# Kernel tuning notes

Measured on AMD Instinct MI355X. Metric: run time of the kernel, lower is better.

The kernel has to match this reference:

```python
import jax, jax.numpy as jnp
import numpy as np

PROJ_DIM = 16384  # self.projDim / output_dim
THRESH = 1e-8     # self.thresh


def setup_inputs() -> dict:
    key = jax.random.key(0)
    k1, k2, k3, k4, k5 = jax.random.split(key, 5)
    B, C, H, W = 16, 2048, 14, 14
    x = jax.random.normal(k1, (B, C, H, W), dtype=jnp.float32)
    # count-sketch hash indices and Rademacher signs (fixed random params of CBP)
    h1 = jax.random.randint(k2, (C,), 0, PROJ_DIM, dtype=jnp.int32)
    h2 = jax.random.randint(k3, (C,), 0, PROJ_DIM, dtype=jnp.int32)
    w1 = (2 * jax.random.randint(k4, (C,), 0, 2) - 1).astype(jnp.float32)
    w2 = (2 * jax.random.randint(k5, (C,), 0, 2) - 1).astype(jnp.float32)
    return {"x": x, "w1": w1, "w2": w2, "h1": h1, "h2": h2}


def _count_sketch(xf, w, h):
    # xf: (N, C); scatter-add signed features into PROJ_DIM bins per location
    N = xf.shape[0]
    return jnp.zeros((N, PROJ_DIM), xf.dtype).at[:, h].add(xf * w)


def reference(x, w1, w2, h1, h2):
    B, C, H, W = x.shape
    # (B, C, H, W) -> (B*H*W, C): one feature vector per spatial location
    xf = x.transpose(0, 2, 3, 1).reshape(B * H * W, C)
    s1 = _count_sketch(xf, w1, h1)  # (N, D)
    s2 = _count_sketch(xf, w2, h2)  # (N, D)
    # circular convolution of the two sketches via FFT (real input -> rfft)
    y = jnp.fft.irfft(jnp.fft.rfft(s1, axis=-1) * jnp.fft.rfft(s2, axis=-1),
                      n=PROJ_DIM, axis=-1)  # (N, D)
    # sum-pool over spatial locations
    y = y.reshape(B, H * W, PROJ_DIM).sum(axis=1)  # (B, D)
    # signed sqrt + L2 normalization
    y = jnp.sign(y) * jnp.sqrt(jnp.abs(y) + THRESH)
    y = y / jnp.sqrt(jnp.sum(y * y, axis=-1, keepdims=True) + THRESH)
    return y  # (B, 16384), already flat as in torch.flatten(..., 1)
```

## Files before the change

kernel.cpp:

```cpp
#include <hip/hip_runtime.h>


#define D_PROJ 16384
#define C_CH   2048
#define HW_N   196
#define NKS    7
#define KPAD   (NKS * 32)
#define B_N    16
#define THREADS 512
#define NT     64
#define BUFS   6
#define AHEAD  4
#define ROWSH  448
#define FPSCALE 65536.0f
#define INVSCALE (1.0f / 65536.0f)

typedef short  short8 __attribute__((ext_vector_type(8)));
typedef float  f32x4  __attribute__((ext_vector_type(4)));
typedef int    i32x4  __attribute__((ext_vector_type(4)));

static __device__ inline unsigned short f2bf(float f) {
    union { float f; unsigned u; } a; a.f = f;
    unsigned u = a.u;
    return (unsigned short)((u + 0x7FFFu + ((u >> 16) & 1u)) >> 16);
}
static __device__ inline float bf2f(unsigned short h) {
    union { unsigned u; float f; } a; a.u = ((unsigned)h) << 16;
    return a.f;
}
static __device__ inline f32x4 mfma16(short8 a, short8 b, f32x4 c) {
    return __builtin_amdgcn_mfma_f32_16x16x32_bf16(a, b, c, 0, 0, 0);
}

static __device__ inline void lds_iadd(int* p, int v) {
    unsigned off = (unsigned)(uintptr_t)p;
    asm volatile("ds_add_u32 %0, %1" :: "v"(off), "v"(v) : "memory");
}
static __device__ inline void lds_fadd(float* p, float v) {
    unsigned off = (unsigned)(uintptr_t)p;
    asm volatile("ds_add_f32 %0, %1" :: "v"(off), "v"(v) : "memory");
}
static __device__ inline void lds_drain() {
    asm volatile("s_waitcnt lgkmcnt(0)" ::: "memory");
    __builtin_amdgcn_sched_barrier(0);
}

static __device__ inline int swz_off(int ks, int lo64, int sub16, int row7) {
    return (((ks << 7) | lo64 | (sub16 << 4)) ^ (row7 << 4));
}

__global__ __launch_bounds__(256)
void cbp_convert(const float* __restrict__ x, unsigned short* __restrict__ ws) {
    const int id = blockIdx.x * 256 + threadIdx.x;
    const int total = B_N * C_CH * (KPAD / 8);
    if (id >= total) return;
    const int row = id / (KPAD / 8);
    const int sub = id - row * (KPAD / 8);
    const int k0  = sub * 8;
    const int ks  = k0 >> 5;
    const int s16 = (k0 >> 3) & 3;

    const float* xr = x + (size_t)row * HW_N;
    float v[8];
    if (k0 + 8 <= HW_N) {
        f32x4 p0 = *(const f32x4*)(xr + k0);
        f32x4 p1 = *(const f32x4*)(xr + k0 + 4);
#pragma unroll
        for (int e = 0; e < 4; ++e) { v[e] = p0[e]; v[4 + e] = p1[e]; }
    } else {
#pragma unroll
        for (int e = 0; e < 8; ++e) {
            const int k = k0 + e;
            v[e] = (k < HW_N) ? xr[k] : 0.0f;
        }
    }
    short8 hv, lv;
#pragma unroll
    for (int e = 0; e < 8; ++e) {
        unsigned short h = f2bf(v[e]);
        hv[e] = (short)h;
        lv[e] = (short)f2bf(v[e] - bf2f(h));
    }
    char* rowB = (char*)ws + (size_t)row * (ROWSH * 2);
    const int r7 = row & 7;
    *(short8*)(rowB + swz_off(ks, 0,  s16, r7)) = hv;
    *(short8*)(rowB + swz_off(ks, 64, s16, r7)) = lv;
}

static __device__ inline void stage_issue(const unsigned short* __restrict__ src0,
                                          unsigned short* dst0, int wave, int lane) {
    if (lane < 56) {
#pragma unroll
        for (int hlf = 0; hlf < 2; ++hlf) {
            const int row = wave + hlf * 8;
            const unsigned short* s = src0 + (size_t)row * ROWSH + (size_t)lane * 8;
            unsigned short* d = dst0 + (size_t)row * ROWSH;
            __builtin_amdgcn_global_load_lds(
                (const __attribute__((address_space(1))) void*)s,
                (__attribute__((address_space(3))) void*)d, 16, 0, 0);
        }
    }
}

__global__ __launch_bounds__(THREADS, 2)
void cbp_gram10(const unsigned short* __restrict__ ws,
                const float* __restrict__ w1f,
                const float* __restrict__ w2f,
                const int*   __restrict__ h1,
                const int*   __restrict__ h2,
                int*         __restrict__ part) {
    __shared__ __align__(16) int hist[D_PROJ];
    __shared__ __align__(16) unsigned short stage[BUFS][16 * ROWSH];
    __shared__ float w2sh[1024];
    __shared__ int   h2sh[1024];

    const int id   = blockIdx.x;
    const int b    = ((id & 7) << 1) | ((id >> 3) & 1);
    const int rest = id >> 4;
    const int j0   = (rest & 1) * 1024;
    const int i0   = (rest >> 1) * 256;

    const int tid  = threadIdx.x;
    const int wave = tid >> 6;
    const int lane = tid & 63;
    const int l15  = lane & 15;
    const int lgrp = lane >> 4;
    const int r7s  = (l15 & 7) << 4;

    for (int t = tid; t < D_PROJ / 4; t += THREADS)
        ((i32x4*)hist)[t] = i32x4{0, 0, 0, 0};
    for (int t = tid; t < 1024; t += THREADS) {
        w2sh[t] = w2f[j0 + t];
        h2sh[t] = h2[j0 + t];
    }

    short8 ah[2][NKS], al[2][NKS];
    int    binr[2][4];
    float  s1r[2][4];
#pragma unroll
    for (int s = 0; s < 2; ++s) {
        const int irow = i0 + wave * 32 + s * 16 + l15;
        const char* rowA = (const char*)(ws + ((size_t)b * C_CH + irow) * ROWSH);
#pragma unroll
        for (int ks = 0; ks < NKS; ++ks) {
            ah[s][ks] = *(const short8*)(rowA + (((ks << 7) | (lgrp << 4)) ^ r7s));
            al[s][ks] = *(const short8*)(rowA + (((ks << 7) | 64 | (lgrp << 4)) ^ r7s));
        }
#pragma unroll
        for (int r = 0; r < 4; ++r) {
            const int ir = i0 + wave * 32 + s * 16 + lgrp * 4 + r;
            binr[s][r] = h1[ir];
            s1r[s][r]  = w1f[ir];
        }
    }

    const unsigned short* jbase = ws + ((size_t)b * C_CH + j0) * ROWSH;
#pragma unroll
    for (int p = 0; p < AHEAD; ++p)
        stage_issue(jbase + (size_t)p * 16 * ROWSH, stage[p], wave, lane);

    asm volatile("s_waitcnt lgkmcnt(0)\ns_barrier" ::: "memory");

    for (int t = 0; t < NT; ++t) {
        int tt = t + AHEAD; tt = (tt < NT) ? tt : (NT - 1);
        stage_issue(jbase + (size_t)tt * 16 * ROWSH, stage[(t + AHEAD) % BUFS], wave, lane);
        asm volatile("s_waitcnt vmcnt(8)" ::: "memory");
        __builtin_amdgcn_sched_barrier(0);
        asm volatile("s_barrier" ::: "memory");
        __builtin_amdgcn_sched_barrier(0);

        const char* srow = (const char*)&stage[t % BUFS][(size_t)l15 * ROWSH];
        f32x4 a0 = {0.f,0.f,0.f,0.f}, a1 = {0.f,0.f,0.f,0.f};
        f32x4 b0 = {0.f,0.f,0.f,0.f}, b1 = {0.f,0.f,0.f,0.f};
#pragma unroll
        for (int ks = 0; ks < NKS; ++ks) {
            const short8 bh = *(const short8*)(srow + (((ks << 7) | (lgrp << 4)) ^ r7s));
            const short8 bl = *(const short8*)(srow + (((ks << 7) | 64 | (lgrp << 4)) ^ r7s));
            if (ks & 1) {
                a1 = mfma16(ah[0][ks], bh, a1);  b1 = mfma16(ah[1][ks], bh, b1);
                a1 = mfma16(al[0][ks], bh, a1);  b1 = mfma16(al[1][ks], bh, b1);
                a1 = mfma16(ah[0][ks], bl, a1);  b1 = mfma16(ah[1][ks], bl, b1);
            } else {
                a0 = mfma16(ah[0][ks], bh, a0);  b0 = mfma16(ah[1][ks], bh, b0);
                a0 = mfma16(al[0][ks], bh, a0);  b0 = mfma16(al[1][ks], bh, b0);
                a0 = mfma16(ah[0][ks], bl, a0);  b0 = mfma16(ah[1][ks], bl, b0);
            }
        }
        const float w2vs = w2sh[t * 16 + l15] * FPSCALE;
        const int   h2v  = h2sh[t * 16 + l15];
        const f32x4 g0 = a0 + a1;
        const f32x4 g1 = b0 + b1;
#pragma unroll
        for (int r = 0; r < 4; ++r) {
            int bin = binr[0][r] + h2v;
            if (bin >= D_PROJ) bin -= D_PROJ;
            const int iv = (int)rintf(g0[r] * (s1r[0][r] * w2vs));
            lds_iadd(&hist[bin], iv);
        }
#pragma unroll
        for (int r = 0; r < 4; ++r) {
            int bin = binr[1][r] + h2v;
            if (bin >= D_PROJ) bin -= D_PROJ;
            const int iv = (int)rintf(g1[r] * (s1r[1][r] * w2vs));
            lds_iadd(&hist[bin], iv);
        }
    }

    lds_drain();
    __syncthreads();
    int* pslot = part + ((size_t)(b * 16 + rest)) * D_PROJ;
    for (int t = tid; t < D_PROJ / 4; t += THREADS)
        ((i32x4*)pslot)[t] = ((const i32x4*)hist)[t];
}

__global__ void cbp_finalize2(const int* __restrict__ part, float* __restrict__ y) {
    const int b   = blockIdx.x;
    const int tid = threadIdx.x;
    const int* pb = part + (size_t)b * 16 * D_PROJ;
    float* yb = y + (size_t)b * D_PROJ;
    __shared__ float partial[4];

    float ssum = 0.f;
    for (int t = tid; t < D_PROJ; t += 256) {
        int acc = 0;
#pragma unroll
        for (int s = 0; s < 16; ++s) acc += pb[(size_t)s * D_PROJ + t];
        float v = (float)acc * INVSCALE;
        float sg = copysignf(sqrtf(fabsf(v) + 1e-8f), v);
        yb[t] = sg;
        ssum += sg * sg;
    }
    const int lane = tid & 63, wv = tid >> 6;
#pragma unroll
    for (int off = 32; off > 0; off >>= 1) ssum += __shfl_down(ssum, off, 64);
    if (lane == 0) partial[wv] = ssum;
    __syncthreads();
    const float total = partial[0] + partial[1] + partial[2] + partial[3];
    const float inv = 1.0f / sqrtf(total + 1e-8f);
    for (int t = tid; t < D_PROJ; t += 256) yb[t] *= inv;
}

static __device__ inline void cvt_split(const float (&v)[8], short8& hi, short8& lo) {
#pragma unroll
    for (int e = 0; e < 8; ++e) {
        unsigned short h = f2bf(v[e]);
        hi[e] = (short)h;
        lo[e] = (short)f2bf(v[e] - bf2f(h));
    }
}

__global__ __launch_bounds__(256, 2)
void cbp_gram_scatter(const float* __restrict__ x,
                      const float* __restrict__ w1f,
                      const float* __restrict__ w2f,
                      const int*   __restrict__ h1,
                      const int*   __restrict__ h2,
                      float*       __restrict__ y) {
    __shared__ float hist[D_PROJ];
    const int b    = blockIdx.y;
    const int i0   = blockIdx.x * 64;
    const int tid  = threadIdx.x;
    const int wave = tid >> 6;
    const int lane = tid & 63;
    const int l15  = lane & 15;
    const int lgrp = lane >> 4;

    for (int t = tid; t < D_PROJ; t += 256) hist[t] = 0.0f;
    const float* xb = x + (size_t)b * (C_CH * HW_N);

    const int    irow = i0 + wave * 16 + l15;
    const float* xa   = xb + (size_t)irow * HW_N;
    const float  w1s  = w1f[irow];
    short8 a_hi[NKS], a_lo[NKS];
#pragma unroll
    for (int ks = 0; ks < NKS; ++ks) {
        const int k0 = ks * 32 + lgrp * 8;
        float v[8];
#pragma unroll
        for (int e = 0; e < 8; ++e) {
            const int k = k0 + e;
            v[e] = (k < HW_N) ? xa[k] * w1s : 0.0f;
        }
        cvt_split(v, a_hi[ks], a_lo[ks]);
    }
    int bin1[4];
#pragma unroll
    for (int r = 0; r < 4; ++r) bin1[r] = h1[i0 + wave * 16 + lgrp * 4 + r];

    __syncthreads();

    for (int jt = 0; jt < C_CH / 16; ++jt) {
        const int    jrow = jt * 16 + l15;
        const float* xj   = xb + (size_t)jrow * HW_N;
        const float  w2s  = w2f[jrow];
        const int    h2j  = h2[jrow];
        f32x4 acc0 = {0.f, 0.f, 0.f, 0.f};
        f32x4 acc1 = {0.f, 0.f, 0.f, 0.f};
#pragma unroll
        for (int ks = 0; ks < NKS; ++ks) {
            const int k0 = ks * 32 + lgrp * 8;
            float v[8];
            if (ks < 6) {
                f32x4 p0 = *(const f32x4*)(xj + k0);
                f32x4 p1 = *(const f32x4*)(xj + k0 + 4);
#pragma unroll
                for (int e = 0; e < 4; ++e) { v[e] = p0[e]; v[4 + e] = p1[e]; }
            } else {
#pragma unroll
                for (int e = 0; e < 8; ++e) {
                    const int k = k0 + e;
                    v[e] = (k < HW_N) ? xj[k] : 0.0f;
                }
            }
#pragma unroll
            for (int e = 0; e < 8; ++e) v[e] *= w2s;
            short8 bhi, blo;
            cvt_split(v, bhi, blo);
            if (ks & 1) {
                acc1 = mfma16(a_hi[ks], bhi, acc1);
                acc1 = mfma16(a_hi[ks], blo, acc1);
                acc1 = mfma16(a_lo[ks], bhi, acc1);
            } else {
                acc0 = mfma16(a_hi[ks], bhi, acc0);
                acc0 = mfma16(a_hi[ks], blo, acc0);
                acc0 = mfma16(a_lo[ks], bhi, acc0);
            }
        }
        const f32x4 g = acc0 + acc1;
#pragma unroll
        for (int r = 0; r < 4; ++r) {
            int bin = bin1[r] + h2j;
            if (bin >= D_PROJ) bin -= D_PROJ;
            lds_fadd(&hist[bin], g[r]);
        }
    }

    lds_drain();
    __syncthreads();
    float* yb = y + (size_t)b * D_PROJ;
    for (int t = tid; t < D_PROJ; t += 256)
        atomicAdd(&yb[t], hist[t]);
}

__global__ void cbp_finalize(float* __restrict__ y) {
    const int b   = blockIdx.x;
    const int tid = threadIdx.x;
    float* yb = y + (size_t)b * D_PROJ;
    __shared__ float partial[4];

    float ssum = 0.f;
    for (int t = tid; t < D_PROJ; t += 256) {
        float v = yb[t];
        float s = copysignf(sqrtf(fabsf(v) + 1e-8f), v);
        yb[t] = s;
        ssum += s * s;
    }
    const int lane = tid & 63, wv = tid >> 6;
#pragma unroll
    for (int off = 32; off > 0; off >>= 1) ssum += __shfl_down(ssum, off, 64);
    if (lane == 0) partial[wv] = ssum;
    __syncthreads();
    const float total = partial[0] + partial[1] + partial[2] + partial[3];
    const float inv = 1.0f / sqrtf(total + 1e-8f);
    for (int t = tid; t < D_PROJ; t += 256) yb[t] *= inv;
}

extern "C" void kernel_launch(void* const* d_in, const int* in_sizes, int n_in,
                              void* d_out, int out_size, void* d_ws, size_t ws_size,
                              hipStream_t stream) {
    const float* x  = (const float*)d_in[0];
    const float* w1 = (const float*)d_in[1];
    const float* w2 = (const float*)d_in[2];
    const int*   h1 = (const int*)d_in[3];
    const int*   h2 = (const int*)d_in[4];
    float* y = (float*)d_out;

    const size_t need = (size_t)B_N * C_CH * ROWSH * 2 * sizeof(unsigned short);
    const size_t planeBytes = (size_t)B_N * C_CH * ROWSH * sizeof(unsigned short);

    if (ws_size >= need) {
        unsigned short* wsp = (unsigned short*)d_ws;
        int* part = (int*)((char*)d_ws + planeBytes);
        const int total = B_N * C_CH * (KPAD / 8);
        cbp_convert<<<(total + 255) / 256, 256, 0, stream>>>(x, wsp);
        cbp_gram10<<<256, THREADS, 0, stream>>>(wsp, w1, w2, h1, h2, part);
        cbp_finalize2<<<B_N, 256, 0, stream>>>(part, y);
    } else {
        hipMemsetAsync(y, 0, (size_t)B_N * D_PROJ * sizeof(float), stream);
        dim3 grid(C_CH / 64, B_N);
        cbp_gram_scatter<<<grid, 256, 0, stream>>>(x, w1, w2, h1, h2, y);
        cbp_finalize<<<B_N, 256, 0, stream>>>(y);
    }
}
```

Measured before the change: 134.5 us.

## Fuse finalize into gram kernel via last-block counter, pair-step staging

Removes the separate finalize launch: each gram block writes its partial histogram, bumps a per-batch atomic counter, and the last of the 16 blocks reduces the partials and applies signed sqrt and L2 normalisation, keeping values in registers. The staging loop now processes two tiles per barrier with prefetch distance two instead of four, halving barriers but lowering the lookahead. The w2 sign is packed into the h2 index word and applied by XOR of the sign bit, saving a multiply and a shared array. A memset for the counters is added, and the finalize work now runs serially inside one block per batch.

```diff
diff --git a/kernel.cpp b/kernel.cpp
--- a/kernel.cpp
+++ b/kernel.cpp
@@ -10,8 +10,8 @@
 #define THREADS 512
 #define NT     64
 #define BUFS   6
-#define AHEAD  4
 #define ROWSH  448
+#define TILE_SH (16 * ROWSH)
 #define FPSCALE 65536.0f
 #define INVSCALE (1.0f / 65536.0f)
 
@@ -103,16 +103,19 @@
 }
 
 __global__ __launch_bounds__(THREADS, 2)
-void cbp_gram10(const unsigned short* __restrict__ ws,
+void cbp_gram11(const unsigned short* __restrict__ ws,
                 const float* __restrict__ w1f,
                 const float* __restrict__ w2f,
                 const int*   __restrict__ h1,
                 const int*   __restrict__ h2,
-                int*         __restrict__ part) {
+                int*         __restrict__ part,
+                int*         __restrict__ cnt,
+                float*       __restrict__ y) {
     __shared__ __align__(16) int hist[D_PROJ];
-    __shared__ __align__(16) unsigned short stage[BUFS][16 * ROWSH];
-    __shared__ float w2sh[1024];
-    __shared__ int   h2sh[1024];
+    __shared__ __align__(16) unsigned short stage[BUFS][TILE_SH];
+    __shared__ int   pairsh[1024];
+    __shared__ float wsum[8];
+    __shared__ int   lastFlag;
 
     const int id   = blockIdx.x;
     const int b    = ((id & 7) << 1) | ((id >> 3) & 1);
@@ -129,14 +132,12 @@
 
     for (int t = tid; t < D_PROJ / 4; t += THREADS)
         ((i32x4*)hist)[t] = i32x4{0, 0, 0, 0};
-    for (int t = tid; t < 1024; t += THREADS) {
-        w2sh[t] = w2f[j0 + t];
-        h2sh[t] = h2[j0 + t];
-    }
+    for (int t = tid; t < 1024; t += THREADS)
+        pairsh[t] = h2[j0 + t] | (w2f[j0 + t] < 0.f ? (int)0x80000000 : 0);
 
     short8 ah[2][NKS], al[2][NKS];
     int    binr[2][4];
-    float  s1r[2][4];
+    float  s1s[2][4];
 #pragma unroll
     for (int s = 0; s < 2; ++s) {
         const int irow = i0 + wave * 32 + s * 16 + l15;
@@ -150,94 +151,113 @@
         for (int r = 0; r < 4; ++r) {
             const int ir = i0 + wave * 32 + s * 16 + lgrp * 4 + r;
             binr[s][r] = h1[ir];
-            s1r[s][r]  = w1f[ir];
+            s1s[s][r]  = w1f[ir] * FPSCALE;
         }
     }
 
     const unsigned short* jbase = ws + ((size_t)b * C_CH + j0) * ROWSH;
-#pragma unroll
-    for (int p = 0; p < AHEAD; ++p)
-        stage_issue(jbase + (size_t)p * 16 * ROWSH, stage[p], wave, lane);
-
+    stage_issue(jbase,               stage[0], wave, lane);
+    stage_issue(jbase + TILE_SH,     stage[1], wave, lane);
     asm volatile("s_waitcnt lgkmcnt(0)\ns_barrier" ::: "memory");
 
-    for (int t = 0; t < NT; ++t) {
-        int tt = t + AHEAD; tt = (tt < NT) ? tt : (NT - 1);
-        stage_issue(jbase + (size_t)tt * 16 * ROWSH, stage[(t + AHEAD) % BUFS], wave, lane);
-        asm volatile("s_waitcnt vmcnt(8)" ::: "memory");
+    int rb = 0, sb = 2;
+    for (int t = 0; t < NT; t += 2) {
+        int t2 = t + 2; if (t2 > NT - 1) t2 = NT - 1;
+        int t3 = t + 3; if (t3 > NT - 1) t3 = NT - 1;
+        stage_issue(jbase + (size_t)t2 * TILE_SH, stage[sb],     wave, lane);
+        stage_issue(jbase + (size_t)t3 * TILE_SH, stage[sb + 1 == BUFS ? 0 : sb + 1], wave, lane);
+        asm volatile("s_waitcnt vmcnt(4)" ::: "memory");
         __builtin_amdgcn_sched_barrier(0);
         asm volatile("s_barrier" ::: "memory");
         __builtin_amdgcn_sched_barrier(0);
 
-        const char* srow = (const char*)&stage[t % BUFS][(size_t)l15 * ROWSH];
-        f32x4 a0 = {0.f,0.f,0.f,0.f}, a1 = {0.f,0.f,0.f,0.f};
-        f32x4 b0 = {0.f,0.f,0.f,0.f}, b1 = {0.f,0.f,0.f,0.f};
-#pragma unroll
-        for (int ks = 0; ks < NKS; ++ks) {
-            const short8 bh = *(const short8*)(srow + (((ks << 7) | (lgrp << 4)) ^ r7s));
-            const short8 bl = *(const short8*)(srow + (((ks << 7) | 64 | (lgrp << 4)) ^ r7s));
-            if (ks & 1) {
-                a1 = mfma16(ah[0][ks], bh, a1);  b1 = mfma16(ah[1][ks], bh, b1);
-                a1 = mfma16(al[0][ks], bh, a1);  b1 = mfma16(al[1][ks], bh, b1);
-                a1 = mfma16(ah[0][ks], bl, a1);  b1 = mfma16(ah[1][ks], bl, b1);
-            } else {
-                a0 = mfma16(ah[0][ks], bh, a0);  b0 = mfma16(ah[1][ks], bh, b0);
-                a0 = mfma16(al[0][ks], bh, a0);  b0 = mfma16(al[1][ks], bh, b0);
-                a0 = mfma16(ah[0][ks], bl, a0);  b0 = mfma16(ah[1][ks], bl, b0);
+#pragma unroll
+        for (int half = 0; half < 2; ++half) {
+            const int tt  = t + half;
+            const int buf = (half == 0) ? rb : (rb + 1 == BUFS ? 0 : rb + 1);
+            const char* srow = (const char*)&stage[buf][(size_t)l15 * ROWSH];
+            f32x4 a0 = {0.f,0.f,0.f,0.f}, a1 = {0.f,0.f,0.f,0.f};
+            f32x4 b0 = {0.f,0.f,0.f,0.f}, b1 = {0.f,0.f,0.f,0.f};
+#pragma unroll
+            for (int ks = 0; ks < NKS; ++ks) {
+                const short8 bh = *(const short8*)(srow + (((ks << 7) | (lgrp << 4)) ^ r7s));
+                const short8 bl = *(const short8*)(srow + (((ks << 7) | 64 | (lgrp << 4)) ^ r7s));
+                if (ks & 1) {
+                    a1 = mfma16(ah[0][ks], bh, a1);  b1 = mfma16(ah[1][ks], bh, b1);
+                    a1 = mfma16(al[0][ks], bh, a1);  b1 = mfma16(al[1][ks], bh, b1);
+                    a1 = mfma16(ah[0][ks], bl, a1);  b1 = mfma16(ah[1][ks], bl, b1);
+                } else {
+                    a0 = mfma16(ah[0][ks], bh, a0);  b0 = mfma16(ah[1][ks], bh, b0);
+                    a0 = mfma16(al[0][ks], bh, a0);  b0 = mfma16(al[1][ks], bh, b0);
+                    a0 = mfma16(ah[0][ks], bl, a0);  b0 = mfma16(ah[1][ks], bl, b0);
+                }
             }
-        }
-        const float w2vs = w2sh[t * 16 + l15] * FPSCALE;
-        const int   h2v  = h2sh[t * 16 + l15];
-        const f32x4 g0 = a0 + a1;
-        const f32x4 g1 = b0 + b1;
-#pragma unroll
-        for (int r = 0; r < 4; ++r) {
-            int bin = binr[0][r] + h2v;
-            if (bin >= D_PROJ) bin -= D_PROJ;
-            const int iv = (int)rintf(g0[r] * (s1r[0][r] * w2vs));
-            lds_iadd(&hist[bin], iv);
-        }
-#pragma unroll
-        for (int r = 0; r < 4; ++r) {
-            int bin = binr[1][r] + h2v;
-            if (bin >= D_PROJ) bin -= D_PROJ;
-            const int iv = (int)rintf(g1[r] * (s1r[1][r] * w2vs));
-            lds_iadd(&hist[bin], iv);
-        }
+            const unsigned pk  = (unsigned)pairsh[tt * 16 + l15];
+            const int      h2v = (int)(pk & 0x3FFFu);
+            const unsigned sg2 = pk & 0x80000000u;
+            const f32x4 g0 = a0 + a1;
+            const f32x4 g1 = b0 + b1;
+#pragma unroll
+            for (int r = 0; r < 4; ++r) {
+                int bin = binr[0][r] + h2v;
+                if (bin >= D_PROJ) bin -= D_PROJ;
+                const float fv = __uint_as_float(__float_as_uint(g0[r] * s1s[0][r]) ^ sg2);
+                lds_iadd(&hist[bin], (int)rintf(fv));
+            }
+#pragma unroll
+            for (int r = 0; r < 4; ++r) {
+                int bin = binr[1][r] + h2v;
+                if (bin >= D_PROJ) bin -= D_PROJ;
+                const float fv = __uint_as_float(__float_as_uint(g1[r] * s1s[1][r]) ^ sg2);
+                lds_iadd(&hist[bin], (int)rintf(fv));
+            }
+        }
+        rb += 2; if (rb >= BUFS) rb -= BUFS;
+        sb += 2; if (sb >= BUFS) sb -= BUFS;
     }
 
     lds_drain();
     __syncthreads();
-    int* pslot = part + ((size_t)(b * 16 + rest)) * D_PROJ;
+    int* pslot = part + (size_t)(b * 16 + rest) * D_PROJ;
     for (int t = tid; t < D_PROJ / 4; t += THREADS)
         ((i32x4*)pslot)[t] = ((const i32x4*)hist)[t];
-}
-
-__global__ void cbp_finalize2(const int* __restrict__ part, float* __restrict__ y) {
-    const int b   = blockIdx.x;
-    const int tid = threadIdx.x;
+
+    __threadfence();
+    __syncthreads();
+    if (tid == 0) {
+        const int old = atomicAdd(&cnt[b], 1);
+        lastFlag = (old == 15);
+    }
+    __syncthreads();
+    if (!lastFlag) return;
+    __threadfence();
+
     const int* pb = part + (size_t)b * 16 * D_PROJ;
     float* yb = y + (size_t)b * D_PROJ;
-    __shared__ float partial[4];
-
+    float sgv[32];
     float ssum = 0.f;
-    for (int t = tid; t < D_PROJ; t += 256) {
+#pragma unroll
+    for (int k = 0; k < 32; ++k) {
+        const int t = tid + k * THREADS;
         int acc = 0;
 #pragma unroll
         for (int s = 0; s < 16; ++s) acc += pb[(size_t)s * D_PROJ + t];
-        float v = (float)acc * INVSCALE;
-        float sg = copysignf(sqrtf(fabsf(v) + 1e-8f), v);
-        yb[t] = sg;
+        const float v  = (float)acc * INVSCALE;
+        const float sg = copysignf(sqrtf(fabsf(v) + 1e-8f), v);
+        sgv[k] = sg;
         ssum += sg * sg;
     }
-    const int lane = tid & 63, wv = tid >> 6;
 #pragma unroll
     for (int off = 32; off > 0; off >>= 1) ssum += __shfl_down(ssum, off, 64);
-    if (lane == 0) partial[wv] = ssum;
-    __syncthreads();
-    const float total = partial[0] + partial[1] + partial[2] + partial[3];
+    if (lane == 0) wsum[wave] = ssum;
+    __syncthreads();
+    float total = 0.f;
+#pragma unroll
+    for (int w = 0; w < 8; ++w) total += wsum[w];
     const float inv = 1.0f / sqrtf(total + 1e-8f);
-    for (int t = tid; t < D_PROJ; t += 256) yb[t] *= inv;
+#pragma unroll
+    for (int k = 0; k < 32; ++k)
+        yb[tid + k * THREADS] = sgv[k] * inv;
 }
 
 static __device__ inline void cvt_split(const float (&v)[8], short8& hi, short8& lo) {
@@ -377,14 +397,16 @@
 
     const size_t need = (size_t)B_N * C_CH * ROWSH * 2 * sizeof(unsigned short);
     const size_t planeBytes = (size_t)B_N * C_CH * ROWSH * sizeof(unsigned short);
+    const size_t partBytes  = (size_t)256 * D_PROJ * sizeof(int);
 
     if (ws_size >= need) {
         unsigned short* wsp = (unsigned short*)d_ws;
         int* part = (int*)((char*)d_ws + planeBytes);
+        int* cnt  = (int*)((char*)d_ws + planeBytes + partBytes);
+        hipMemsetAsync(cnt, 0, B_N * sizeof(int), stream);
         const int total = B_N * C_CH * (KPAD / 8);
         cbp_convert<<<(total + 255) / 256, 256, 0, stream>>>(x, wsp);
-        cbp_gram10<<<256, THREADS, 0, stream>>>(wsp, w1, w2, h1, h2, part);
-        cbp_finalize2<<<B_N, 256, 0, stream>>>(part, y);
+        cbp_gram11<<<256, THREADS, 0, stream>>>(wsp, w1, w2, h1, h2, part, cnt, y);
     } else {
         hipMemsetAsync(y, 0, (size_t)B_N * D_PROJ * sizeof(float), stream);
         dim3 grid(C_CH / 64, B_N);
```

Result: slower. 164.1 us (+22.0%).

## Process two staged tiles per barrier and pack hash/sign into one word

Applied to the files above, without the earlier changes.

The gram kernel loop now handles two 16-row tiles per iteration. That halves the number of s_barrier/vmcnt waits, and the prefetch of the next two tiles is issued after compute rather than before it. The w2 sign and h2 bin are packed into one int in LDS, and w1 is prescaled by FPSCALE, so the per-element scaling becomes a sign-bit XOR instead of a multiply. The risk is a reduced effective prefetch distance, since the loads are issued later with a vmcnt(4) wait, plus the correctness of the buffer indexing across the 6-buffer ring.

```diff
diff --git a/kernel.cpp b/kernel.cpp
--- a/kernel.cpp
+++ b/kernel.cpp
@@ -10,8 +10,8 @@
 #define THREADS 512
 #define NT     64
 #define BUFS   6
-#define AHEAD  4
 #define ROWSH  448
+#define TILE_SH (16 * ROWSH)
 #define FPSCALE 65536.0f
 #define INVSCALE (1.0f / 65536.0f)
 
@@ -103,16 +103,15 @@
 }
 
 __global__ __launch_bounds__(THREADS, 2)
-void cbp_gram10(const unsigned short* __restrict__ ws,
+void cbp_gram12(const unsigned short* __restrict__ ws,
                 const float* __restrict__ w1f,
                 const float* __restrict__ w2f,
                 const int*   __restrict__ h1,
                 const int*   __restrict__ h2,
                 int*         __restrict__ part) {
     __shared__ __align__(16) int hist[D_PROJ];
-    __shared__ __align__(16) unsigned short stage[BUFS][16 * ROWSH];
-    __shared__ float w2sh[1024];
-    __shared__ int   h2sh[1024];
+    __shared__ __align__(16) unsigned short stage[BUFS][TILE_SH];
+    __shared__ int pairsh[1024];
 
     const int id   = blockIdx.x;
     const int b    = ((id & 7) << 1) | ((id >> 3) & 1);
@@ -129,14 +128,12 @@
 
     for (int t = tid; t < D_PROJ / 4; t += THREADS)
         ((i32x4*)hist)[t] = i32x4{0, 0, 0, 0};
-    for (int t = tid; t < 1024; t += THREADS) {
-        w2sh[t] = w2f[j0 + t];
-        h2sh[t] = h2[j0 + t];
-    }
+    for (int t = tid; t < 1024; t += THREADS)
+        pairsh[t] = h2[j0 + t] | (w2f[j0 + t] < 0.f ? (int)0x80000000 : 0);
 
     short8 ah[2][NKS], al[2][NKS];
     int    binr[2][4];
-    float  s1r[2][4];
+    float  s1s[2][4];
 #pragma unroll
     for (int s = 0; s < 2; ++s) {
         const int irow = i0 + wave * 32 + s * 16 + l15;
@@ -150,65 +147,74 @@
         for (int r = 0; r < 4; ++r) {
             const int ir = i0 + wave * 32 + s * 16 + lgrp * 4 + r;
             binr[s][r] = h1[ir];
-            s1r[s][r]  = w1f[ir];
+            s1s[s][r]  = w1f[ir] * FPSCALE;
         }
     }
 
     const unsigned short* jbase = ws + ((size_t)b * C_CH + j0) * ROWSH;
 #pragma unroll
-    for (int p = 0; p < AHEAD; ++p)
-        stage_issue(jbase + (size_t)p * 16 * ROWSH, stage[p], wave, lane);
-
-    asm volatile("s_waitcnt lgkmcnt(0)\ns_barrier" ::: "memory");
-
-    for (int t = 0; t < NT; ++t) {
-        int tt = t + AHEAD; tt = (tt < NT) ? tt : (NT - 1);
-        stage_issue(jbase + (size_t)tt * 16 * ROWSH, stage[(t + AHEAD) % BUFS], wave, lane);
-        asm volatile("s_waitcnt vmcnt(8)" ::: "memory");
+    for (int p = 0; p < 4; ++p)
+        stage_issue(jbase + (size_t)p * TILE_SH, stage[p], wave, lane);
+    asm volatile("s_waitcnt lgkmcnt(0)" ::: "memory");
+
+    for (int t = 0; t < NT; t += 2) {
+        asm volatile("s_waitcnt vmcnt(4)" ::: "memory");
         __builtin_amdgcn_sched_barrier(0);
         asm volatile("s_barrier" ::: "memory");
         __builtin_amdgcn_sched_barrier(0);
 
-        const char* srow = (const char*)&stage[t % BUFS][(size_t)l15 * ROWSH];
-        f32x4 a0 = {0.f,0.f,0.f,0.f}, a1 = {0.f,0.f,0.f,0.f};
-        f32x4 b0 = {0.f,0.f,0.f,0.f}, b1 = {0.f,0.f,0.f,0.f};
-#pragma unroll
-        for (int ks = 0; ks < NKS; ++ks) {
-            const short8 bh = *(const short8*)(srow + (((ks << 7) | (lgrp << 4)) ^ r7s));
-            const short8 bl = *(const short8*)(srow + (((ks << 7) | 64 | (lgrp << 4)) ^ r7s));
-            if (ks & 1) {
-                a1 = mfma16(ah[0][ks], bh, a1);  b1 = mfma16(ah[1][ks], bh, b1);
-                a1 = mfma16(al[0][ks], bh, a1);  b1 = mfma16(al[1][ks], bh, b1);
-                a1 = mfma16(ah[0][ks], bl, a1);  b1 = mfma16(ah[1][ks], bl, b1);
-            } else {
-                a0 = mfma16(ah[0][ks], bh, a0);  b0 = mfma16(ah[1][ks], bh, b0);
-                a0 = mfma16(al[0][ks], bh, a0);  b0 = mfma16(al[1][ks], bh, b0);
-                a0 = mfma16(ah[0][ks], bl, a0);  b0 = mfma16(ah[1][ks], bl, b0);
+        const int rb = t % BUFS;
+#pragma unroll
+        for (int half = 0; half < 2; ++half) {
+            const int tt  = t + half;
+            const char* srow = (const char*)&stage[rb + half][(size_t)l15 * ROWSH];
+            f32x4 a0 = {0.f,0.f,0.f,0.f}, a1 = {0.f,0.f,0.f,0.f};
+            f32x4 b0 = {0.f,0.f,0.f,0.f}, b1 = {0.f,0.f,0.f,0.f};
+#pragma unroll
+            for (int ks = 0; ks < NKS; ++ks) {
+                const short8 bh = *(const short8*)(srow + (((ks << 7) | (lgrp << 4)) ^ r7s));
+                const short8 bl = *(const short8*)(srow + (((ks << 7) | 64 | (lgrp << 4)) ^ r7s));
+                if (ks & 1) {
+                    a1 = mfma16(ah[0][ks], bh, a1);  b1 = mfma16(ah[1][ks], bh, b1);
+                    a1 = mfma16(al[0][ks], bh, a1);  b1 = mfma16(al[1][ks], bh, b1);
+                    a1 = mfma16(ah[0][ks], bl, a1);  b1 = mfma16(ah[1][ks], bl, b1);
+                } else {
+                    a0 = mfma16(ah[0][ks], bh, a0);  b0 = mfma16(ah[1][ks], bh, b0);
+                    a0 = mfma16(al[0][ks], bh, a0);  b0 = mfma16(al[1][ks], bh, b0);
+                    a0 = mfma16(ah[0][ks], bl, a0);  b0 = mfma16(ah[1][ks], bl, b0);
+                }
             }
-        }
-        const float w2vs = w2sh[t * 16 + l15] * FPSCALE;
-        const int   h2v  = h2sh[t * 16 + l15];
-        const f32x4 g0 = a0 + a1;
-        const f32x4 g1 = b0 + b1;
-#pragma unroll
-        for (int r = 0; r < 4; ++r) {
-            int bin = binr[0][r] + h2v;
-            if (bin >= D_PROJ) bin -= D_PROJ;
-            const int iv = (int)rintf(g0[r] * (s1r[0][r] * w2vs));
-            lds_iadd(&hist[bin], iv);
-        }
-#pragma unroll
-        for (int r = 0; r < 4; ++r) {
-            int bin = binr[1][r] + h2v;
-            if (bin >= D_PROJ) bin -= D_PROJ;
-            const int iv = (int)rintf(g1[r] * (s1r[1][r] * w2vs));
-            lds_iadd(&hist[bin], iv);
-        }
+            const unsigned pk  = (unsigned)pairsh[tt * 16 + l15];
+            const int      h2v = (int)(pk & 0x3FFFu);
+            const unsigned sg2 = pk & 0x80000000u;
+            const f32x4 g0 = a0 + a1;
+            const f32x4 g1 = b0 + b1;
+#pragma unroll
+            for (int r = 0; r < 4; ++r) {
+                int bin = binr[0][r] + h2v;
+                if (bin >= D_PROJ) bin -= D_PROJ;
+                const float fv = __uint_as_float(__float_as_uint(g0[r] * s1s[0][r]) ^ sg2);
+                lds_iadd(&hist[bin], (int)rintf(fv));
+            }
+#pragma unroll
+            for (int r = 0; r < 4; ++r) {
+                int bin = binr[1][r] + h2v;
+                if (bin >= D_PROJ) bin -= D_PROJ;
+                const float fv = __uint_as_float(__float_as_uint(g1[r] * s1s[1][r]) ^ sg2);
+                lds_iadd(&hist[bin], (int)rintf(fv));
+            }
+        }
+
+        int t4 = t + 4; if (t4 > NT - 1) t4 = NT - 1;
+        int t5 = t + 5; if (t5 > NT - 1) t5 = NT - 1;
+        const int sb = (t + 4) % BUFS;
+        stage_issue(jbase + (size_t)t4 * TILE_SH, stage[sb],     wave, lane);
+        stage_issue(jbase + (size_t)t5 * TILE_SH, stage[sb + 1], wave, lane);
     }
 
     lds_drain();
     __syncthreads();
-    int* pslot = part + ((size_t)(b * 16 + rest)) * D_PROJ;
+    int* pslot = part + (size_t)(b * 16 + rest) * D_PROJ;
     for (int t = tid; t < D_PROJ / 4; t += THREADS)
         ((i32x4*)pslot)[t] = ((const i32x4*)hist)[t];
 }
@@ -383,7 +389,7 @@
         int* part = (int*)((char*)d_ws + planeBytes);
         const int total = B_N * C_CH * (KPAD / 8);
         cbp_convert<<<(total + 255) / 256, 256, 0, stream>>>(x, wsp);
-        cbp_gram10<<<256, THREADS, 0, stream>>>(wsp, w1, w2, h1, h2, part);
+        cbp_gram12<<<256, THREADS, 0, stream>>>(wsp, w1, w2, h1, h2, part);
         cbp_finalize2<<<B_N, 256, 0, stream>>>(part, y);
     } else {
         hipMemsetAsync(y, 0, (size_t)B_N * D_PROJ * sizeof(float), stream);
```

Result: no change. 132.5 us (-1.5%).
